# Performance work log

Measured on AMD Instinct MI355X. Metric: run time of the kernel, lower is better.

## Reference

```python
import jax, jax.numpy as jnp
import numpy as np

NUM_USERS = 100000
NUM_ITEMS = 200000
N = NUM_USERS + NUM_ITEMS
D = 64
NNZ = 5_000_000
B = 16384
N_LAYERS = 3


def setup_inputs() -> dict:
    key = jax.random.key(0)
    ks = jax.random.split(key, 7)
    users = jax.random.randint(ks[0], (B,), 0, NUM_USERS, dtype=jnp.int32)
    items = jax.random.randint(ks[1], (B,), 0, NUM_ITEMS, dtype=jnp.int32)
    edge_row = jax.random.randint(ks[2], (NNZ,), 0, N, dtype=jnp.int32)
    edge_col = jax.random.randint(ks[3], (NNZ,), 0, N, dtype=jnp.int32)
    # mimic D^-1/2 A D^-1/2 normalization scale (~1/avg_degree)
    edge_vals = jax.random.uniform(ks[4], (NNZ,), dtype=jnp.float32) * 0.06
    user_emb = jax.random.normal(ks[5], (NUM_USERS, D), dtype=jnp.float32) * 0.1
    item_emb = jax.random.normal(ks[6], (NUM_ITEMS, D), dtype=jnp.float32) * 0.1
    return {
        "users": users, "items": items,
        "edge_row": edge_row, "edge_col": edge_col, "edge_vals": edge_vals,
        "user_emb": user_emb, "item_emb": item_emb,
        "n_layers": N_LAYERS,
    }


def _spmm(edge_row, edge_col, edge_vals, x):
    # sparse [N,N] @ dense [N,D] via gather + segment_sum
    msg = x[edge_col] * edge_vals[:, None]  # [nnz, D]
    return jax.ops.segment_sum(msg, edge_row, num_segments=N)


def reference(users, items, edge_row, edge_col, edge_vals, user_emb, item_emb, n_layers):
    # LightGCN.computer(): propagate + mean over layers (running-sum form)
    all_emb = jnp.concatenate([user_emb, item_emb], axis=0)  # [N, D]
    acc = all_emb
    for _ in range(n_layers):
        all_emb = _spmm(edge_row, edge_col, edge_vals, all_emb)
        acc = acc + all_emb
    light_out = acc / (n_layers + 1)
    all_users = light_out[:NUM_USERS]
    all_items = light_out[NUM_USERS:]
    # forward(users, items): elementwise dot product
    users_emb = all_users[users]
    items_emb = all_items[items]
    gamma = jnp.sum(users_emb * items_emb, axis=1)  # [B]
    return gamma
```

## Files before the change

kernel.cpp:

```cpp
#include <hip/hip_runtime.h>
#include <hip/hip_fp16.h>
#include <hip/hip_fp8.h>

namespace {

constexpr int kUsers = 100000;
constexpr int kItems = 200000;
constexpr int kN     = kUsers + kItems;
constexpr int kD     = 64;
constexpr int kNNZ   = 5000000;
constexpr int kB     = 16384;
constexpr int kRowsPerBkt = 2048;
constexpr int kNBKT  = (kN + kRowsPerBkt - 1) / kRowsPerBkt;
constexpr int kSEPB  = 4096;
constexpr int kCap   = 40960;
constexpr int kMaxSub = 2 * kB;

typedef int   v2i __attribute__((ext_vector_type(2)));
typedef float v4f __attribute__((ext_vector_type(4)));

#if defined(__has_builtin)
#if __has_builtin(__builtin_amdgcn_cvt_pk_f32_fp8) && __has_builtin(__builtin_amdgcn_cvt_f32_fp8)
#define NATIVE_FP8 1
#endif
#endif
#ifndef NATIVE_FP8
#define NATIVE_FP8 0
#endif

constexpr float kValScale = NATIVE_FP8 ? 1.0f : 256.0f;

__device__ inline void dec8(v2i h, float* f) {
#if NATIVE_FP8
  auto a0 = __builtin_amdgcn_cvt_pk_f32_fp8(h.x, false);
  auto a1 = __builtin_amdgcn_cvt_pk_f32_fp8(h.x, true);
  auto a2 = __builtin_amdgcn_cvt_pk_f32_fp8(h.y, false);
  auto a3 = __builtin_amdgcn_cvt_pk_f32_fp8(h.y, true);
  f[0] = a0[0]; f[1] = a0[1]; f[2] = a1[0]; f[3] = a1[1];
  f[4] = a2[0]; f[5] = a2[1]; f[6] = a3[0]; f[7] = a3[1];
#else
  unsigned int ws[2] = {(unsigned int)h.x, (unsigned int)h.y};
#pragma unroll
  for (int q = 0; q < 2; ++q) {
    unsigned int w = ws[q];
    unsigned int a = ((w & 0x007f007fu) << 7) | ((w & 0x00800080u) << 8);
    unsigned int b = (((w >> 8) & 0x007f007fu) << 7) | (((w >> 8) & 0x00800080u) << 8);
    float2 e = __half22float2(*reinterpret_cast<const __half2*>(&a));
    float2 o = __half22float2(*reinterpret_cast<const __half2*>(&b));
    f[4 * q + 0] = e.x; f[4 * q + 1] = o.x; f[4 * q + 2] = e.y; f[4 * q + 3] = o.y;
  }
#endif
}

__device__ inline float dec1(unsigned char b) {
#if NATIVE_FP8
  return __builtin_amdgcn_cvt_f32_fp8((int)b, 0) * 0.015625f;
#else
  unsigned int hb = ((b & 0x7fu) << 7) | ((b & 0x80u) << 8);
  return __half2float(__ushort_as_half((unsigned short)hb)) * 4.0f;
#endif
}

__device__ inline unsigned char enc(float f) { __hip_fp8_e4m3 q(f); return q.__x; }

__device__ inline float vdec(int w) {
  return __half2float(__ushort_as_half((unsigned short)((w >> 17) & 0x7FFC))) * kValScale;
}

__global__ void zero3(int* __restrict__ gpos, int* __restrict__ mark,
                      int* __restrict__ dh, int* __restrict__ scnt) {
  int i = blockIdx.x * blockDim.x + threadIdx.x;
  if (i < kN) mark[i] = 0;
  if (i < kNBKT + 1) gpos[i] = 0;
  if (i < 64) dh[i] = 0;
  if (i == 0) scnt[0] = 0;
}

__global__ void bucket_scatter(const int* __restrict__ row, const int* __restrict__ col,
                               const float* __restrict__ val, int* __restrict__ gpos,
                               int* __restrict__ tmp4, unsigned short* __restrict__ tmpr) {
  __shared__ int hcnt[4][kNBKT];
  __shared__ int lofs[kNBKT];
  __shared__ int hbase[kNBKT];
  __shared__ int lds[256];
  __shared__ int sp[kSEPB];
  __shared__ unsigned short sr[kSEPB];
  __shared__ unsigned short sb[kSEPB];
  int t = threadIdx.x;
  int wv = t >> 6;
  long base = (long)blockIdx.x * kSEPB;
  int valid = (int)min((long)kSEPB, (long)kNNZ - base);
  for (int i = t; i < kNBKT; i += 256) {
    hcnt[0][i] = 0; hcnt[1][i] = 0; hcnt[2][i] = 0; hcnt[3][i] = 0;
  }
  __syncthreads();
  int py[16], bk[16], rl[16], rk[16];
  bool ok[16];
#pragma unroll
  for (int j = 0; j < 16; ++j) {
    long i = base + j * 256 + t;
    ok[j] = (i < kNNZ);
    if (ok[j]) {
      int r = __builtin_nontemporal_load(row + i);
      int c = __builtin_nontemporal_load(col + i);
      float v = __builtin_nontemporal_load(val + i);
      bk[j] = r >> 11;
      rl[j] = r & 2047;
      unsigned short hb = __half_as_ushort(__float2half_rn(v));
      int v13 = ((int)hb + 2) >> 2;
      py[j] = c | (v13 << 19);
      rk[j] = atomicAdd(&hcnt[wv][bk[j]], 1);
    }
  }
  __syncthreads();
  int own = 0;
  if (t < kNBKT) {
    int c0 = hcnt[0][t], c1 = hcnt[1][t], c2 = hcnt[2][t], c3 = hcnt[3][t];
    hcnt[0][t] = 0; hcnt[1][t] = c0; hcnt[2][t] = c0 + c1; hcnt[3][t] = c0 + c1 + c2;
    own = c0 + c1 + c2 + c3;
  }
  lds[t] = own;
  __syncthreads();
  for (int o = 1; o < 256; o <<= 1) {
    int x = (t >= o) ? lds[t - o] : 0;
    __syncthreads();
    if (t >= o) lds[t] += x;
    __syncthreads();
  }
  if (t < kNBKT) {
    lofs[t] = lds[t] - own;
    hbase[t] = t * kCap + atomicAdd(&gpos[t], own);
  }
  __syncthreads();
#pragma unroll
  for (int j = 0; j < 16; ++j) {
    if (ok[j]) {
      int pos = lofs[bk[j]] + hcnt[wv][bk[j]] + rk[j];
      sp[pos] = py[j];
      sr[pos] = (unsigned short)rl[j];
      sb[pos] = (unsigned short)bk[j];
    }
  }
  __syncthreads();
#pragma unroll
  for (int j = 0; j < 16; ++j) {
    int pos = t + j * 256;
    if (pos < valid) {
      int b = sb[pos];
      int w = hbase[b] + (pos - lofs[b]);
      tmp4[w] = sp[pos];
      tmpr[w] = sr[pos];
    }
  }
}

__global__ void hist_scan(const int* __restrict__ gpos,
                          const unsigned short* __restrict__ tmpr,
                          int* __restrict__ rowptr, int* __restrict__ partials) {
  __shared__ int h[kRowsPerBkt];
  __shared__ int lsum[256];
  int b = blockIdx.x, t = threadIdx.x;
  for (int i = t; i < kRowsPerBkt; i += 256) h[i] = 0;
  __syncthreads();
  int s = b * kCap;
  int e = s + gpos[b];
  for (int j = s + t; j < e; j += 256) atomicAdd(&h[tmpr[j]], 1);
  __syncthreads();
  int cnt[8], pref[8];
  int acc = 0;
#pragma unroll
  for (int k = 0; k < 8; ++k) {
    cnt[k] = h[t * 8 + k];
    pref[k] = acc;
    acc += cnt[k];
  }
  lsum[t] = acc;
  __syncthreads();
  for (int o = 1; o < 256; o <<= 1) {
    int v = (t >= o) ? lsum[t - o] : 0;
    __syncthreads();
    if (t >= o) lsum[t] += v;
    __syncthreads();
  }
  int ex = (t == 0) ? 0 : lsum[t - 1];
#pragma unroll
  for (int k = 0; k < 8; ++k) {
    int r = b * kRowsPerBkt + t * 8 + k;
    if (r < kN) rowptr[r] = ex + pref[k];
  }
  if (t == 255) partials[b] = lsum[255];
}

__global__ void scan2(int* __restrict__ partials) {
  __shared__ int lds[256];
  int t = threadIdx.x;
  lds[t] = (t < kNBKT) ? partials[t] : 0;
  __syncthreads();
  for (int o = 1; o < 256; o <<= 1) {
    int v = (t >= o) ? lds[t - o] : 0;
    __syncthreads();
    if (t >= o) lds[t] += v;
    __syncthreads();
  }
  int ex = (t == 0) ? 0 : lds[t - 1];
  if (t < kNBKT) partials[t] = ex;
}

__global__ void scan3(int* __restrict__ rowptr, const int* __restrict__ partials) {
  int i = blockIdx.x * blockDim.x + threadIdx.x;
  if (i < kN) rowptr[i] += partials[i >> 11];
  else if (i == kN) rowptr[kN] = kNNZ;
}

__global__ __launch_bounds__(1024) void place(
    const int* __restrict__ gpos, const int* __restrict__ tmp4,
    const unsigned short* __restrict__ tmpr, const int* __restrict__ rowptr,
    int* __restrict__ edges) {
  __shared__ int rank[kRowsPerBkt];
  int b = blockIdx.x, t = threadIdx.x;
  for (int i = t; i < kRowsPerBkt; i += 1024) rank[i] = 0;
  __syncthreads();
  int s = b * kCap;
  int e = s + gpos[b];
  const int* rp = rowptr + b * kRowsPerBkt;
  for (int j = s + t; j < e; j += 1024) {
    int pay = tmp4[j];
    int rl = tmpr[j];
    int k = atomicAdd(&rank[rl], 1);
    edges[rp[rl] + k] = pay;
  }
}

__global__ void mark_rows(const int* __restrict__ users, const int* __restrict__ items,
                          int* __restrict__ mark) {
  int i = blockIdx.x * blockDim.x + threadIdx.x;
  if (i >= kB) return;
  mark[users[i]] = 1;
  mark[kUsers + items[i]] = 1;
}

__global__ void sub_hist(const int* __restrict__ rowptr, const int* __restrict__ mark,
                         int* __restrict__ dh) {
  __shared__ int h[64];
  int t = threadIdx.x;
  if (t < 64) h[t] = 0;
  __syncthreads();
  int i = blockIdx.x * 256 + t;
  if (i < kN && mark[i]) {
    int d = min(rowptr[i + 1] - rowptr[i], 63);
    atomicAdd(&h[d], 1);
  }
  __syncthreads();
  if (t < 64 && h[t]) atomicAdd(&dh[t], h[t]);
}

__global__ void deg_scan(int* __restrict__ dh, int* __restrict__ scnt) {
  int t = threadIdx.x;
  int v = dh[t];
  int x = v;
  for (int o = 1; o < 64; o <<= 1) {
    int y = __shfl_up(x, o, 64);
    if (t >= o) x += y;
  }
  if (t == 63) *scnt = x;
  dh[t] = x - v;
}

__global__ void sub_place(const int* __restrict__ rowptr, const int* __restrict__ mark,
                          int* __restrict__ dh, int* __restrict__ list) {
  __shared__ int h[64], base[64];
  int t = threadIdx.x;
  if (t < 64) h[t] = 0;
  __syncthreads();
  int i = blockIdx.x * 256 + t;
  int d = 0, lr = 0;
  bool okv = (i < kN) && mark[i];
  if (okv) {
    d = min(rowptr[i + 1] - rowptr[i], 63);
    lr = atomicAdd(&h[d], 1);
  }
  __syncthreads();
  if (t < 64) base[t] = h[t] ? atomicAdd(&dh[t], h[t]) : 0;
  __syncthreads();
  if (okv) list[base[d] + lr] = i;
}

__global__ void mark_cols(const int* __restrict__ list, const int* __restrict__ cnt,
                          const int* __restrict__ rowptr, const int* __restrict__ edges,
                          int* __restrict__ mark) {
  int p = blockIdx.x * blockDim.x + threadIdx.x;
  if (p >= *cnt) return;
  int r = list[p];
  int s = rowptr[r], e = rowptr[r + 1];
  for (int j = s; j < e; ++j) mark[edges[j] & 0x7FFFF] = 1;
}

__global__ void to_fp8(const float* __restrict__ ue, const float* __restrict__ ie,
                       unsigned char* __restrict__ xq) {
  int t = blockIdx.x * blockDim.x + threadIdx.x;
  if (t >= kN * kD / 8) return;
  int row = t >> 3;
  int seg = t & 7;
  const float* src = (row < kUsers) ? (ue + (size_t)row * kD + seg * 8)
                                    : (ie + (size_t)(row - kUsers) * kD + seg * 8);
  v4f a = __builtin_nontemporal_load((const v4f*)src);
  v4f b = __builtin_nontemporal_load((const v4f*)src + 1);
  float f[8] = {a.x, a.y, a.z, a.w, b.x, b.y, b.z, b.w};
  unsigned int w0 = 0, w1 = 0;
#pragma unroll
  for (int k = 0; k < 4; ++k) w0 |= (unsigned int)enc(f[k] * 64.f) << (8 * k);
#pragma unroll
  for (int k = 0; k < 4; ++k) w1 |= (unsigned int)enc(f[4 + k] * 64.f) << (8 * k);
  v2i o; o.x = (int)w0; o.y = (int)w1;
  ((v2i*)xq)[t] = o;
}

template <int MODE>
__global__ __launch_bounds__(256, 8) void spmm(
    const int* __restrict__ rowptr, const int* __restrict__ edges,
    const unsigned char* __restrict__ x, unsigned char* __restrict__ yq,
    const int* __restrict__ aux, const int* __restrict__ cnt) {
  int t = threadIdx.x;
  int l = t & 7;
  int wid = (blockIdx.x * 256 + t) >> 6;
  int g = (t >> 3) & 7;
  int p = wid * 8 + g;
  int r = -1;
  bool live = false;
  if (MODE == 2) {
    int n = *cnt;
    if (p < n) { r = aux[p]; live = true; }
  } else {
    if (p < kN) { r = p; live = (MODE == 0) || (aux[r] != 0); }
  }
  int s = 0, e = 0;
  if (live) { s = rowptr[r]; e = rowptr[r + 1]; }
  int mx = e - s;
#pragma unroll
  for (int m = 8; m <= 32; m <<= 1) mx = max(mx, __shfl_xor(mx, m, 64));
  float acc[8];
#pragma unroll
  for (int k = 0; k < 8; ++k) acc[k] = 0.f;
  int last = max(e - 1, 0);
  int j = s;
  int E0 = edges[min(j, last)];
  int E1 = edges[min(j + 1, last)];
  int E2 = edges[min(j + 2, last)];
  int E3 = edges[min(j + 3, last)];
  for (int it = 0; it < mx; it += 4) {
    float v0 = (j     < e) ? vdec(E0) : 0.f;
    float v1 = (j + 1 < e) ? vdec(E1) : 0.f;
    float v2 = (j + 2 < e) ? vdec(E2) : 0.f;
    float v3 = (j + 3 < e) ? vdec(E3) : 0.f;
    v2i h0 = ((const v2i*)(x + (size_t)(E0 & 0x7FFFF) * kD))[l];
    v2i h1 = ((const v2i*)(x + (size_t)(E1 & 0x7FFFF) * kD))[l];
    v2i h2 = ((const v2i*)(x + (size_t)(E2 & 0x7FFFF) * kD))[l];
    v2i h3 = ((const v2i*)(x + (size_t)(E3 & 0x7FFFF) * kD))[l];
    j += 4;
    E0 = edges[min(j, last)];
    E1 = edges[min(j + 1, last)];
    E2 = edges[min(j + 2, last)];
    E3 = edges[min(j + 3, last)];
    float f[8];
    dec8(h0, f);
#pragma unroll
    for (int k = 0; k < 8; ++k) acc[k] = fmaf(v0, f[k], acc[k]);
    dec8(h1, f);
#pragma unroll
    for (int k = 0; k < 8; ++k) acc[k] = fmaf(v1, f[k], acc[k]);
    dec8(h2, f);
#pragma unroll
    for (int k = 0; k < 8; ++k) acc[k] = fmaf(v2, f[k], acc[k]);
    dec8(h3, f);
#pragma unroll
    for (int k = 0; k < 8; ++k) acc[k] = fmaf(v3, f[k], acc[k]);
  }
  if (live) {
    unsigned int w0 = 0, w1 = 0;
#pragma unroll
    for (int k = 0; k < 4; ++k) w0 |= (unsigned int)enc(acc[k]) << (8 * k);
#pragma unroll
    for (int k = 0; k < 4; ++k) w1 |= (unsigned int)enc(acc[4 + k]) << (8 * k);
    v2i o; o.x = (int)w0; o.y = (int)w1;
    ((v2i*)yq)[(size_t)r * 8 + l] = o;
  }
}

__global__ void acc_add_init(const int* __restrict__ users, const int* __restrict__ items,
                             const float* __restrict__ uemb, const float* __restrict__ iemb,
                             const unsigned char* __restrict__ xq, float* __restrict__ uacc,
                             float* __restrict__ iacc) {
  int tid = blockIdx.x * blockDim.x + threadIdx.x;
  if (tid >= kB * kD) return;
  int b = tid >> 6, d = tid & 63;
  int u = users[b], iw = items[b];
  uacc[tid] = uemb[(size_t)u * kD + d] + dec1(xq[(size_t)u * kD + d]);
  iacc[tid] = iemb[(size_t)iw * kD + d] + dec1(xq[(size_t)(kUsers + iw) * kD + d]);
}

__global__ void acc_add(const int* __restrict__ users, const int* __restrict__ items,
                        const unsigned char* __restrict__ xq, float* __restrict__ uacc,
                        float* __restrict__ iacc) {
  int tid = blockIdx.x * blockDim.x + threadIdx.x;
  if (tid >= kB * kD) return;
  int b = tid >> 6, d = tid & 63;
  uacc[tid] += dec1(xq[(size_t)users[b] * kD + d]);
  iacc[tid] += dec1(xq[(size_t)(kUsers + items[b]) * kD + d]);
}

__global__ void acc_add_fin(const int* __restrict__ users, const int* __restrict__ items,
                            const unsigned char* __restrict__ xq, const float* __restrict__ uacc,
                            const float* __restrict__ iacc, float* __restrict__ out) {
  int tid = blockIdx.x * blockDim.x + threadIdx.x;
  if (tid >= kB * kD) return;
  int b = tid >> 6, d = tid & 63;
  float u = uacc[tid] + dec1(xq[(size_t)users[b] * kD + d]);
  float v = iacc[tid] + dec1(xq[(size_t)(kUsers + items[b]) * kD + d]);
  float p = u * v;
  for (int o = 32; o > 0; o >>= 1) p += __shfl_down(p, o, 64);
  if (d == 0) out[b] = p * 0.0625f;
}

}

extern "C" void kernel_launch(void* const* d_in, const int* in_sizes, int n_in,
                              void* d_out, int out_size, void* d_ws, size_t ws_size,
                              hipStream_t stream) {
  const int*   users = (const int*)d_in[0];
  const int*   items = (const int*)d_in[1];
  const int*   erow  = (const int*)d_in[2];
  const int*   ecol  = (const int*)d_in[3];
  const float* evals = (const float*)d_in[4];
  const float* uemb  = (const float*)d_in[5];
  const float* iemb  = (const float*)d_in[6];
  float* out = (float*)d_out;

  char* ws = (char*)d_ws;
  size_t off = 0;
  auto take = [&](size_t bytes) -> char* {
    char* p = ws + off;
    off = (off + bytes + 255) & ~(size_t)255;
    return p;
  };
  int*    rowptr   = (int*)take((size_t)(kN + 1) * 4);
  int*    gpos     = (int*)take((kNBKT + 1) * 4);
  int*    partials = (int*)take(256 * 4);
  int*    dh       = (int*)take(256 * 4);
  int*    mark     = (int*)take((size_t)kN * 4);
  int*    list     = (int*)take((size_t)kMaxSub * 4);
  int*    scnt     = (int*)take(256);
  int*    edges    = (int*)take((size_t)kNNZ * 4);
  int*    tmp4     = (int*)take((size_t)kNBKT * kCap * 4);
  unsigned short* tmpr = (unsigned short*)take((size_t)kNBKT * kCap * 2);
  unsigned char* xq0 = (unsigned char*)take((size_t)kN * kD);
  unsigned char* xq1 = (unsigned char*)take((size_t)kN * kD);
  float*  uacc     = (float*)take((size_t)kB * kD * 4);
  float*  iacc     = (float*)take((size_t)kB * kD * 4);
  (void)ws_size; (void)in_sizes; (void)n_in; (void)out_size;

  const int nScatBlocks = (kNNZ + kSEPB - 1) / kSEPB;
  const int nSpmmBlocks = (kN + 31) / 32;
  const int nSubBlocks  = (kMaxSub + 31) / 32;
  const int nRowBlocks  = (kN + 255) / 256;

  zero3<<<nRowBlocks, 256, 0, stream>>>(gpos, mark, dh, scnt);
  bucket_scatter<<<nScatBlocks, 256, 0, stream>>>(erow, ecol, evals, gpos, tmp4, tmpr);
  hist_scan<<<kNBKT, 256, 0, stream>>>(gpos, tmpr, rowptr, partials);
  scan2<<<1, 256, 0, stream>>>(partials);
  scan3<<<(kN + 1 + 255) / 256, 256, 0, stream>>>(rowptr, partials);
  place<<<kNBKT, 1024, 0, stream>>>(gpos, tmp4, tmpr, rowptr, edges);

  mark_rows<<<(kB + 255) / 256, 256, 0, stream>>>(users, items, mark);
  sub_hist<<<nRowBlocks, 256, 0, stream>>>(rowptr, mark, dh);
  deg_scan<<<1, 64, 0, stream>>>(dh, scnt);
  sub_place<<<nRowBlocks, 256, 0, stream>>>(rowptr, mark, dh, list);
  mark_cols<<<(kMaxSub + 255) / 256, 256, 0, stream>>>(list, scnt, rowptr, edges, mark);

  to_fp8<<<(kN * kD / 8 + 255) / 256, 256, 0, stream>>>(uemb, iemb, xq0);
  spmm<0><<<nSpmmBlocks, 256, 0, stream>>>(rowptr, edges, xq0, xq1, nullptr, nullptr);
  acc_add_init<<<(kB * kD) / 256, 256, 0, stream>>>(users, items, uemb, iemb, xq1, uacc, iacc);
  spmm<1><<<nSpmmBlocks, 256, 0, stream>>>(rowptr, edges, xq1, xq0, mark, nullptr);
  acc_add<<<(kB * kD) / 256, 256, 0, stream>>>(users, items, xq0, uacc, iacc);
  spmm<2><<<nSubBlocks, 256, 0, stream>>>(rowptr, edges, xq0, xq1, list, scnt);
  acc_add_fin<<<(kB * kD) / 256, 256, 0, stream>>>(users, items, xq1, uacc, iacc, out);
}
```

Measured before the change: 519.2 us.

## Fuse CSR histogram, scans and placement into a single build kernel

Merges hist_scan, scan2, scan3 and place into one build_csr kernel. Each block scans the per-bucket counts (gpos) itself to get its global base offset. It then histograms its rows, turns the local prefix into global rowptr entries, and places edges through atomic cursors in LDS. This removes three launches and the second pass over tmp4/tmpr metadata and rowptr. In exchange every block redundantly scans the 147 bucket counts.

```diff
diff --git a/kernel.cpp b/kernel.cpp
--- a/kernel.cpp
+++ b/kernel.cpp
@@ -154,80 +154,65 @@
   }
 }
 
-__global__ void hist_scan(const int* __restrict__ gpos,
-                          const unsigned short* __restrict__ tmpr,
-                          int* __restrict__ rowptr, int* __restrict__ partials) {
+__global__ __launch_bounds__(1024) void build_csr(
+    const int* __restrict__ gpos, const int* __restrict__ tmp4,
+    const unsigned short* __restrict__ tmpr, int* __restrict__ rowptr,
+    int* __restrict__ edges) {
   __shared__ int h[kRowsPerBkt];
   __shared__ int lsum[256];
+  __shared__ int gscan[256];
   int b = blockIdx.x, t = threadIdx.x;
-  for (int i = t; i < kRowsPerBkt; i += 256) h[i] = 0;
-  __syncthreads();
+  if (t < 256) gscan[t] = (t < kNBKT) ? gpos[t] : 0;
+  for (int i = t; i < kRowsPerBkt; i += 1024) h[i] = 0;
+  __syncthreads();
+  for (int o = 1; o < 256; o <<= 1) {
+    int v = 0;
+    if (t < 256 && t >= o) v = gscan[t - o];
+    __syncthreads();
+    if (t < 256 && t >= o) gscan[t] += v;
+    __syncthreads();
+  }
+  int bucket_base = (b == 0) ? 0 : gscan[b - 1];
   int s = b * kCap;
   int e = s + gpos[b];
-  for (int j = s + t; j < e; j += 256) atomicAdd(&h[tmpr[j]], 1);
+  for (int j = s + t; j < e; j += 1024) atomicAdd(&h[tmpr[j]], 1);
   __syncthreads();
   int cnt[8], pref[8];
-  int acc = 0;
-#pragma unroll
-  for (int k = 0; k < 8; ++k) {
-    cnt[k] = h[t * 8 + k];
-    pref[k] = acc;
-    acc += cnt[k];
-  }
-  lsum[t] = acc;
+  if (t < 256) {
+    int acc = 0;
+#pragma unroll
+    for (int k = 0; k < 8; ++k) {
+      cnt[k] = h[t * 8 + k];
+      pref[k] = acc;
+      acc += cnt[k];
+    }
+    lsum[t] = acc;
+  }
   __syncthreads();
   for (int o = 1; o < 256; o <<= 1) {
-    int v = (t >= o) ? lsum[t - o] : 0;
-    __syncthreads();
-    if (t >= o) lsum[t] += v;
-    __syncthreads();
-  }
-  int ex = (t == 0) ? 0 : lsum[t - 1];
-#pragma unroll
-  for (int k = 0; k < 8; ++k) {
-    int r = b * kRowsPerBkt + t * 8 + k;
-    if (r < kN) rowptr[r] = ex + pref[k];
-  }
-  if (t == 255) partials[b] = lsum[255];
-}
-
-__global__ void scan2(int* __restrict__ partials) {
-  __shared__ int lds[256];
-  int t = threadIdx.x;
-  lds[t] = (t < kNBKT) ? partials[t] : 0;
-  __syncthreads();
-  for (int o = 1; o < 256; o <<= 1) {
-    int v = (t >= o) ? lds[t - o] : 0;
-    __syncthreads();
-    if (t >= o) lds[t] += v;
-    __syncthreads();
-  }
-  int ex = (t == 0) ? 0 : lds[t - 1];
-  if (t < kNBKT) partials[t] = ex;
-}
-
-__global__ void scan3(int* __restrict__ rowptr, const int* __restrict__ partials) {
-  int i = blockIdx.x * blockDim.x + threadIdx.x;
-  if (i < kN) rowptr[i] += partials[i >> 11];
-  else if (i == kN) rowptr[kN] = kNNZ;
-}
-
-__global__ __launch_bounds__(1024) void place(
-    const int* __restrict__ gpos, const int* __restrict__ tmp4,
-    const unsigned short* __restrict__ tmpr, const int* __restrict__ rowptr,
-    int* __restrict__ edges) {
-  __shared__ int rank[kRowsPerBkt];
-  int b = blockIdx.x, t = threadIdx.x;
-  for (int i = t; i < kRowsPerBkt; i += 1024) rank[i] = 0;
-  __syncthreads();
-  int s = b * kCap;
-  int e = s + gpos[b];
-  const int* rp = rowptr + b * kRowsPerBkt;
+    int v = 0;
+    if (t < 256 && t >= o) v = lsum[t - o];
+    __syncthreads();
+    if (t < 256 && t >= o) lsum[t] += v;
+    __syncthreads();
+  }
+  if (t < 256) {
+    int ex = (t == 0) ? 0 : lsum[t - 1];
+#pragma unroll
+    for (int k = 0; k < 8; ++k) {
+      int g = bucket_base + ex + pref[k];
+      int r = b * kRowsPerBkt + t * 8 + k;
+      if (r < kN) rowptr[r] = g;
+      h[t * 8 + k] = g;
+    }
+  }
+  if (b == kNBKT - 1 && t == 0) rowptr[kN] = kNNZ;
+  __syncthreads();
   for (int j = s + t; j < e; j += 1024) {
     int pay = tmp4[j];
     int rl = tmpr[j];
-    int k = atomicAdd(&rank[rl], 1);
-    edges[rp[rl] + k] = pay;
+    int dst = atomicAdd(&h[rl], 1);
+    edges[dst] = pay;
   }
 }
 
@@ -444,7 +429,6 @@
   };
   int*    rowptr   = (int*)take((size_t)(kN + 1) * 4);
   int*    gpos     = (int*)take((kNBKT + 1) * 4);
-  int*    partials = (int*)take(256 * 4);
   int*    dh       = (int*)take(256 * 4);
   int*    mark     = (int*)take((size_t)kN * 4);
   int*    list     = (int*)take((size_t)kMaxSub * 4);
@@ -465,10 +449,7 @@
 
   zero3<<<nRowBlocks, 256, 0, stream>>>(gpos, mark, dh, scnt);
   bucket_scatter<<<nScatBlocks, 256, 0, stream>>>(erow, ecol, evals, gpos, tmp4, tmpr);
-  hist_scan<<<kNBKT, 256, 0, stream>>>(gpos, tmpr, rowptr, partials);
-  scan2<<<1, 256, 0, stream>>>(partials);
-  scan3<<<(kN + 1 + 255) / 256, 256, 0, stream>>>(rowptr, partials);
-  place<<<kNBKT, 1024, 0, stream>>>(gpos, tmp4, tmpr, rowptr, edges);
+  build_csr<<<kNBKT, 1024, 0, stream>>>(gpos, tmp4, tmpr, rowptr, edges);
 
   mark_rows<<<(kB + 255) / 256, 256, 0, stream>>>(users, items, mark);
   sub_hist<<<nRowBlocks, 256, 0, stream>>>(rowptr, mark, dh);
```

Result: faster. 483.0 us (-7.0%).
